# Kernel tuning notes

Measured on AMD Instinct MI355X. Metric: run time of the kernel, lower is better.

Reference implementation:

```python
import jax, jax.numpy as jnp
import numpy as np

EMB = 256
IN_CH = 256
CTX_D = 128


def setup_inputs() -> dict:
    key = jax.random.key(0)
    ks = jax.random.split(key, 12)
    b, c, h, w = 16, IN_CH, 48, 48
    seq = 2048
    s = 0.02
    return {
        "x": jax.random.normal(ks[0], (b, c, h, w), jnp.float32),
        "context": jax.random.normal(ks[1], (b, seq, CTX_D), jnp.float32),
        "pad_mask": jax.random.bernoulli(ks[2], 0.1, (b, h * w, seq)),
        "W_in": jax.random.normal(ks[3], (EMB, IN_CH), jnp.float32) * s,   # 1x1 conv weight
        "b_in": jnp.zeros((EMB,), jnp.float32),
        "Wq": jax.random.normal(ks[4], (EMB, EMB), jnp.float32) * s,
        "bq": jnp.zeros((EMB,), jnp.float32),
        "Wk": jax.random.normal(ks[5], (EMB, CTX_D), jnp.float32) * s,
        "bk": jnp.zeros((EMB,), jnp.float32),
        "Wv": jax.random.normal(ks[6], (EMB, CTX_D), jnp.float32) * s,
        "bv": jnp.zeros((EMB,), jnp.float32),
        "W_out": jax.random.normal(ks[7], (IN_CH, EMB), jnp.float32) * s,  # 1x1 conv weight
        "b_out": jnp.zeros((IN_CH,), jnp.float32),
    }


def reference(x, context, pad_mask, W_in, b_in, Wq, bq, Wk, bk, Wv, bv, W_out, b_out):
    b, c, h, w = x.shape
    scale = EMB ** (-0.5)
    # proj_in: 1x1 conv == channel matmul; then b c h w -> b (h w) c
    xt = jnp.einsum('bchw,ec->behw', x, W_in) + b_in[None, :, None, None]
    xt = xt.reshape(b, EMB, h * w).transpose(0, 2, 1)          # [b, hw, emb]
    Q = xt @ Wq.T + bq                                          # [b, hw, emb]
    K = context @ Wk.T + bk                                     # [b, seq, emb]
    V = context @ Wv.T + bv                                     # [b, seq, emb]
    att = jnp.einsum('bid,bjd->bij', Q, K) * scale              # [b, hw, seq]
    att = jnp.where(pad_mask, jnp.float32(-1e9), att)
    att = jax.nn.softmax(att, axis=-1)
    out = jnp.einsum('bij,bjd->bid', att, V)                    # [b, hw, emb]
    out = out.transpose(0, 2, 1).reshape(b, EMB, h, w)
    out = jnp.einsum('behw,ce->bchw', out, W_out) + b_out[None, :, None, None]
    return out, att
```

## Files before the change

kernel.cpp:

```cpp
#include <hip/hip_runtime.h>

typedef unsigned short u16;
typedef unsigned int   u32;
typedef __attribute__((ext_vector_type(8))) __bf16 bf16x8;
typedef __attribute__((ext_vector_type(4))) float  f32x4;

#define BB   16
#define CH   256
#define HW   2304
#define SEQ  2048
#define EMB  256
#define CTXD 128
#define OUT0 9437184
#define NQT  72
#define SLOTF 65536

#define MFMA(a,b,c) __builtin_amdgcn_mfma_f32_16x16x32_bf16(a,b,c,0,0,0)

__device__ __forceinline__ u16 f2bf(float f){
  u32 u = __builtin_bit_cast(u32, f);
  u += 0x7fffu + ((u >> 16) & 1u);
  return (u16)(u >> 16);
}
__device__ __forceinline__ float bf2f(u32 us){ return __builtin_bit_cast(float, us << 16); }

__device__ __forceinline__ bf16x8 ld16(const u16* p){
  uint4 q = *reinterpret_cast<const uint4*>(p);
  return __builtin_bit_cast(bf16x8, q);
}
__device__ __forceinline__ bf16x8 mk8(float a0,float a1,float a2,float a3,
                                      float a4,float a5,float a6,float a7){
  uint4 q;
  q.x = (u32)f2bf(a0) | ((u32)f2bf(a1) << 16);
  q.y = (u32)f2bf(a2) | ((u32)f2bf(a3) << 16);
  q.z = (u32)f2bf(a4) | ((u32)f2bf(a5) << 16);
  q.w = (u32)f2bf(a6) | ((u32)f2bf(a7) << 16);
  return __builtin_bit_cast(bf16x8, q);
}

__global__ __launch_bounds__(256) void k_prep(
    const float* __restrict__ Wq, const float* __restrict__ W_in,
    const float* __restrict__ b_in, const float* __restrict__ bq,
    const float* __restrict__ Wk, const float* __restrict__ Wv,
    const float* __restrict__ Wout,
    u16* __restrict__ WqinBf, u16* __restrict__ WkBf, u16* __restrict__ WvBf,
    u16* __restrict__ WoutBf, float* __restrict__ bq_eff)
{
  int blk = blockIdx.x, t = threadIdx.x;
  if (blk < 256) {
    int e = blk, c = t;
    float s = 0.f;
    for (int f = 0; f < 256; f++) s += Wq[e*256+f] * W_in[f*256+c];
    WqinBf[e*256+c] = f2bf(s);
    if (t == 0) {
      float bb = bq[e];
      for (int f = 0; f < 256; f++) bb += Wq[e*256+f] * b_in[f];
      bq_eff[e] = bb;
    }
  } else {
    u32 flat = (u32)(blk - 256) * 256 + t;
    for (u32 idx = flat; idx < 131072u; idx += 16384u) {
      if (idx < 32768u)       WkBf[idx]          = f2bf(Wk[idx]);
      else if (idx < 65536u)  WvBf[idx - 32768u] = f2bf(Wv[idx - 32768u]);
      else                    WoutBf[idx - 65536u] = f2bf(Wout[idx - 65536u]);
    }
  }
}

__global__ __launch_bounds__(256) void k_qproj(
    const float* __restrict__ x, const u16* __restrict__ WqinBf,
    const float* __restrict__ bq_eff, u16* __restrict__ Qbf)
{
  int b = blockIdx.y, ibase = blockIdx.x * 64;
  int t = threadIdx.x, wv = t >> 6, lane = t & 63, g4 = lane >> 4, r16 = lane & 15;
  int e0 = wv * 64;
  f32x4 acc[4][4] = {};
  #pragma unroll 2
  for (int kk = 0; kk < 8; kk++) {
    bf16x8 a[4];
    #pragma unroll
    for (int m = 0; m < 4; m++)
      a[m] = ld16(WqinBf + (size_t)(e0 + m*16 + r16) * 256 + kk*32 + g4*8);
    bf16x8 bb[4];
    #pragma unroll
    for (int n = 0; n < 4; n++) {
      const float* xp = x + ((size_t)b*CH + kk*32 + g4*8) * HW + ibase + n*16 + r16;
      bb[n] = mk8(xp[0], xp[HW], xp[2*HW], xp[3*HW], xp[4*HW], xp[5*HW], xp[6*HW], xp[7*HW]);
    }
    #pragma unroll
    for (int m = 0; m < 4; m++)
      #pragma unroll
      for (int n = 0; n < 4; n++)
        acc[m][n] = MFMA(a[m], bb[n], acc[m][n]);
  }
  #pragma unroll
  for (int m = 0; m < 4; m++) {
    int e = e0 + m*16 + g4*4;
    float b0 = bq_eff[e], b1 = bq_eff[e+1], b2 = bq_eff[e+2], b3 = bq_eff[e+3];
    #pragma unroll
    for (int n = 0; n < 4; n++) {
      int i = ibase + n*16 + r16;
      u32 lo = (u32)f2bf(acc[m][n][0] + b0) | ((u32)f2bf(acc[m][n][1] + b1) << 16);
      u32 hi = (u32)f2bf(acc[m][n][2] + b2) | ((u32)f2bf(acc[m][n][3] + b3) << 16);
      *(uint2*)(Qbf + ((size_t)b*HW + i) * EMB + e) = make_uint2(lo, hi);
    }
  }
}

__global__ __launch_bounds__(512) void k_kvproj(
    const float* __restrict__ ctx, const u16* __restrict__ WkBf, const u16* __restrict__ WvBf,
    const float* __restrict__ bk, const float* __restrict__ bv,
    u16* __restrict__ Kbf, u16* __restrict__ Vtb)
{
  int b = blockIdx.y, sbase = blockIdx.x * 64;
  int t = threadIdx.x, wv = t >> 6, lane = t & 63, g4 = lane >> 4, r16 = lane & 15;
  bool isV = wv >= 4;
  int e0 = (wv & 3) * 64;
  const u16* Wsel = isV ? WvBf : WkBf;
  f32x4 acc[4][4] = {};
  #pragma unroll
  for (int kk = 0; kk < 4; kk++) {
    bf16x8 a[4];
    #pragma unroll
    for (int m = 0; m < 4; m++)
      a[m] = ld16(Wsel + (size_t)(e0 + m*16 + r16) * 128 + kk*32 + g4*8);
    bf16x8 bb[4];
    #pragma unroll
    for (int n = 0; n < 4; n++) {
      const float* cp = ctx + ((size_t)b*SEQ + sbase + n*16 + r16) * CTXD + kk*32 + g4*8;
      float4 lo = *(const float4*)cp;
      float4 hi = *(const float4*)(cp + 4);
      bb[n] = mk8(lo.x, lo.y, lo.z, lo.w, hi.x, hi.y, hi.z, hi.w);
    }
    #pragma unroll
    for (int m = 0; m < 4; m++)
      #pragma unroll
      for (int n = 0; n < 4; n++)
        acc[m][n] = MFMA(a[m], bb[n], acc[m][n]);
  }
  if (!isV) {
    #pragma unroll
    for (int m = 0; m < 4; m++) {
      int e = e0 + m*16 + g4*4;
      float b0 = bk[e], b1 = bk[e+1], b2 = bk[e+2], b3 = bk[e+3];
      #pragma unroll
      for (int n = 0; n < 4; n++) {
        int s = sbase + n*16 + r16;
        u32 lo = (u32)f2bf(acc[m][n][0] + b0) | ((u32)f2bf(acc[m][n][1] + b1) << 16);
        u32 hi = (u32)f2bf(acc[m][n][2] + b2) | ((u32)f2bf(acc[m][n][3] + b3) << 16);
        *(uint2*)(Kbf + ((size_t)b*SEQ + s) * EMB + e) = make_uint2(lo, hi);
      }
    }
  } else {
    #pragma unroll
    for (int m = 0; m < 4; m++) {
      #pragma unroll
      for (int r = 0; r < 4; r++) {
        int e = e0 + m*16 + g4*4 + r;
        float bvv = bv[e];
        #pragma unroll
        for (int n = 0; n < 4; n++) {
          int s = sbase + n*16 + r16;
          Vtb[((size_t)b*EMB + e) * SEQ + s] = f2bf(acc[m][n][r] + bvv);
        }
      }
    }
  }
}

__global__ __launch_bounds__(512) void k_attn(
    const u16* __restrict__ Qbf, const u16* __restrict__ Kbf,
    const u16* __restrict__ Vtb, const int* __restrict__ mask,
    float* __restrict__ dout, u16* __restrict__ Obf)
{
  __shared__ u16 Els[32][2048];
  __shared__ float red[8][32];
  __shared__ float invs[32];

  int b = blockIdx.y, qt = blockIdx.x, qbase = qt * 32;
  int t = threadIdx.x, wv = t >> 6, lane = t & 63, g4 = lane >> 4, r16 = lane & 15;
  int jb = wv * 256;
  int slot = b * NQT + qt;
  float* attf = dout + OUT0 + (size_t)slot * SLOTF;

  bf16x8 qf[2][8];
  #pragma unroll
  for (int m = 0; m < 2; m++) {
    const u16* qp = Qbf + ((size_t)b*HW + qbase + m*16 + r16) * EMB + g4*8;
    #pragma unroll
    for (int kk = 0; kk < 8; kk++) qf[m][kk] = ld16(qp + kk*32);
  }
  float rs[2][4] = {};
  const float SC = 0.0625f;
  #pragma unroll 1
  for (int nch = 0; nch < 4; nch++) {
    f32x4 acc[2][4] = {};
    #pragma unroll
    for (int kk = 0; kk < 8; kk++) {
      bf16x8 kf[4];
      #pragma unroll
      for (int n = 0; n < 4; n++)
        kf[n] = ld16(Kbf + ((size_t)b*SEQ + jb + nch*64 + n*16 + r16) * EMB + kk*32 + g4*8);
      #pragma unroll
      for (int m = 0; m < 2; m++)
        #pragma unroll
        for (int n = 0; n < 4; n++)
          acc[m][n] = MFMA(qf[m][kk], kf[n], acc[m][n]);
    }
    #pragma unroll
    for (int m = 0; m < 2; m++) {
      int li0 = m*16 + g4*4;
      #pragma unroll
      for (int n = 0; n < 4; n++) {
        int j = jb + nch*64 + n*16 + r16;
        const int* mp = mask + ((size_t)b*HW + qbase + li0) * SEQ + j;
        #pragma unroll
        for (int r = 0; r < 4; r++) {
          float s = acc[m][n][r] * SC;
          int mk = mp[(size_t)r * SEQ];
          float e = mk ? 0.f : __expf(s);
          rs[m][r] += e;
          int row = li0 + r;
          u32 bo = (u32)(j * 2) ^ ((u32)(row & 7) << 4);
          *(u16*)((char*)&Els[row][0] + bo) = f2bf(e);
        }
      }
    }
  }
  #pragma unroll
  for (int m = 0; m < 2; m++)
    #pragma unroll
    for (int r = 0; r < 4; r++) {
      float v = rs[m][r];
      v += __shfl_xor(v, 1); v += __shfl_xor(v, 2);
      v += __shfl_xor(v, 4); v += __shfl_xor(v, 8);
      if (r16 == 0) red[wv][m*16 + g4*4 + r] = v;
    }
  __syncthreads();
  if (t < 32) {
    float s2 = 0.f;
    #pragma unroll
    for (int w2 = 0; w2 < 8; w2++) s2 += red[w2][t];
    invs[t] = 1.f / s2;
  }
  __syncthreads();

  int e0 = wv * 32;
  const u16* Vb = Vtb + (size_t)b * EMB * SEQ;
  int arow = t >> 4;
  int acol = (t & 15) * 2;
  float ivA = invs[arow];
  const char* ErowA = (const char*)&Els[arow][0];
  u32 axor = (u32)(arow & 7) << 4;
  const char* E0p = (const char*)&Els[r16][0];
  const char* E1p = (const char*)&Els[16 + r16][0];
  u32 rxor = (u32)(r16 & 7) << 4;

  f32x4 acc2[2][2] = {};
  #pragma unroll 2
  for (int kk = 0; kk < 64; kk++) {
    int ko = kk*32 + g4*8;
    u32 bo = (u32)(ko * 2) ^ rxor;
    bf16x8 a0 = __builtin_bit_cast(bf16x8, *(const uint4*)(E0p + bo));
    bf16x8 a1 = __builtin_bit_cast(bf16x8, *(const uint4*)(E1p + bo));
    bf16x8 b0 = ld16(Vb + (size_t)(e0 + r16) * SEQ + ko);
    bf16x8 b1 = ld16(Vb + (size_t)(e0 + 16 + r16) * SEQ + ko);
    acc2[0][0] = MFMA(a0, b0, acc2[0][0]);
    acc2[0][1] = MFMA(a0, b1, acc2[0][1]);
    acc2[1][0] = MFMA(a1, b0, acc2[1][0]);
    acc2[1][1] = MFMA(a1, b1, acc2[1][1]);
    u32 abo = (u32)(kk*64 + (t & 15)*4) ^ axor;
    u32 araw = *(const u32*)(ErowA + abo);
    float2 av;
    av.x = bf2f(araw & 0xffffu) * ivA;
    av.y = bf2f(araw >> 16) * ivA;
    *(float2*)(attf + (size_t)arow * 2048 + kk*32 + acol) = av;
  }
  #pragma unroll
  for (int m = 0; m < 2; m++)
    #pragma unroll
    for (int r = 0; r < 4; r++) {
      int li = m*16 + g4*4 + r;
      float iv = invs[li];
      #pragma unroll
      for (int n = 0; n < 2; n++)
        Obf[((size_t)b*HW + qbase + li) * EMB + e0 + n*16 + r16] = f2bf(acc2[m][n][r] * iv);
    }
}

__global__ __launch_bounds__(256) void k_outproj(
    const u16* __restrict__ Obf, const u16* __restrict__ WoutBf,
    const float* __restrict__ bout, float* __restrict__ out)
{
  int b = blockIdx.y, ibase = blockIdx.x * 64;
  int t = threadIdx.x, wv = t >> 6, lane = t & 63, g4 = lane >> 4, r16 = lane & 15;
  int c0 = wv * 64;
  f32x4 acc[4][4] = {};
  #pragma unroll 2
  for (int kk = 0; kk < 8; kk++) {
    bf16x8 a[4];
    #pragma unroll
    for (int m = 0; m < 4; m++)
      a[m] = ld16(WoutBf + (size_t)(c0 + m*16 + r16) * 256 + kk*32 + g4*8);
    bf16x8 bb[4];
    #pragma unroll
    for (int n = 0; n < 4; n++)
      bb[n] = ld16(Obf + ((size_t)b*HW + ibase + n*16 + r16) * EMB + kk*32 + g4*8);
    #pragma unroll
    for (int m = 0; m < 4; m++)
      #pragma unroll
      for (int n = 0; n < 4; n++)
        acc[m][n] = MFMA(a[m], bb[n], acc[m][n]);
  }
  #pragma unroll
  for (int m = 0; m < 4; m++) {
    #pragma unroll
    for (int r = 0; r < 4; r++) {
      int c = c0 + m*16 + g4*4 + r;
      float bo = bout[c];
      #pragma unroll
      for (int n = 0; n < 4; n++) {
        int i = ibase + n*16 + r16;
        out[((size_t)b*CH + c) * HW + i] = acc[m][n][r] + bo;
      }
    }
  }
}

extern "C" void kernel_launch(void* const* d_in, const int* in_sizes, int n_in,
                              void* d_out, int out_size, void* d_ws, size_t ws_size,
                              hipStream_t stream)
{
  const float* x    = (const float*)d_in[0];
  const float* ctx  = (const float*)d_in[1];
  const int*   mask = (const int*)  d_in[2];
  const float* W_in = (const float*)d_in[3];
  const float* b_in = (const float*)d_in[4];
  const float* Wq   = (const float*)d_in[5];
  const float* bq   = (const float*)d_in[6];
  const float* Wk   = (const float*)d_in[7];
  const float* bk   = (const float*)d_in[8];
  const float* Wv   = (const float*)d_in[9];
  const float* bv   = (const float*)d_in[10];
  const float* Wout = (const float*)d_in[11];
  const float* bout = (const float*)d_in[12];
  float* out = (float*)d_out;

  char* ws = (char*)d_ws;
  size_t off = 0;
  auto alloc = [&](size_t bytes) -> void* {
    void* p = ws + off;
    off += (bytes + 255) & ~(size_t)255;
    return p;
  };
  u16*   WqinBf = (u16*)  alloc(256*256*2);
  u16*   WkBf   = (u16*)  alloc(256*128*2);
  u16*   WvBf   = (u16*)  alloc(256*128*2);
  u16*   WoutBf = (u16*)  alloc(256*256*2);
  float* bq_eff = (float*)alloc(256*4);
  u16*   Qbf    = (u16*)  alloc((size_t)BB*HW*EMB*2);
  u16*   Kbf    = (u16*)  alloc((size_t)BB*SEQ*EMB*2);
  u16*   Vtb    = (u16*)  alloc((size_t)BB*EMB*SEQ*2);
  if (off > ws_size) return;

  k_prep<<<dim3(320), dim3(256), 0, stream>>>(Wq, W_in, b_in, bq, Wk, Wv, Wout,
                                              WqinBf, WkBf, WvBf, WoutBf, bq_eff);
  k_qproj<<<dim3(36, 16), dim3(256), 0, stream>>>(x, WqinBf, bq_eff, Qbf);
  k_kvproj<<<dim3(32, 16), dim3(512), 0, stream>>>(ctx, WkBf, WvBf, bk, bv, Kbf, Vtb);
  k_attn<<<dim3(NQT, 16), dim3(512), 0, stream>>>(Qbf, Kbf, Vtb, mask, out, Qbf );
  k_outproj<<<dim3(36, 16), dim3(256), 0, stream>>>(Qbf , WoutBf, bout, out);
}
```

Measured before the change: 502.3 us.

## Pack mask to bits and split attention across 1024-thread blocks

Adds a pre-pass that compresses the int32 pad mask into 64-bit ballot words, so the attention kernel reads bitmasks instead of strided int loads. The attention kernel now runs 16 waves per block, with each wave covering half as many keys and output columns. Q is reloaded per k-step rather than held in registers, and the normalized attention-matrix writeback moves after the PV loop as wide float4 stores. The extra pass still reads the full mask once, and the 1024-thread blocks may limit occupancy.

```diff
diff --git a/kernel.cpp b/kernel.cpp
--- a/kernel.cpp
+++ b/kernel.cpp
@@ -2,6 +2,7 @@
 
 typedef unsigned short u16;
 typedef unsigned int   u32;
+typedef unsigned long long u64;
 typedef __attribute__((ext_vector_type(8))) __bf16 bf16x8;
 typedef __attribute__((ext_vector_type(4))) float  f32x4;
 
@@ -14,6 +15,7 @@
 #define OUT0 9437184
 #define NQT  72
 #define SLOTF 65536
+#define NMASKW 1179648u
 
 #define MFMA(a,b,c) __builtin_amdgcn_mfma_f32_16x16x32_bf16(a,b,c,0,0,0)
 
@@ -67,6 +69,19 @@
   }
 }
 
+__global__ __launch_bounds__(256) void k_maskpack(
+    const int* __restrict__ mask, u64* __restrict__ mb)
+{
+  u32 wid = ((u32)blockIdx.x * 256u + (u32)threadIdx.x) >> 6;
+  u32 lane = threadIdx.x & 63;
+  u32 nwv = ((u32)gridDim.x * 256u) >> 6;
+  for (u32 w = wid; w < NMASKW; w += nwv) {
+    int m = mask[(size_t)w * 64 + lane];
+    u64 bm = __ballot(m != 0);
+    if (lane == 0) mb[w] = bm;
+  }
+}
+
 __global__ __launch_bounds__(256) void k_qproj(
     const float* __restrict__ x, const u16* __restrict__ WqinBf,
     const float* __restrict__ bq_eff, u16* __restrict__ Qbf)
@@ -168,56 +183,60 @@
   }
 }
 
-__global__ __launch_bounds__(512) void k_attn(
+__global__ __launch_bounds__(1024) void k_attn(
     const u16* __restrict__ Qbf, const u16* __restrict__ Kbf,
-    const u16* __restrict__ Vtb, const int* __restrict__ mask,
+    const u16* __restrict__ Vtb, const u32* __restrict__ mb,
     float* __restrict__ dout, u16* __restrict__ Obf)
 {
   __shared__ u16 Els[32][2048];
-  __shared__ float red[8][32];
+  __shared__ float red[16][32];
   __shared__ float invs[32];
 
   int b = blockIdx.y, qt = blockIdx.x, qbase = qt * 32;
   int t = threadIdx.x, wv = t >> 6, lane = t & 63, g4 = lane >> 4, r16 = lane & 15;
-  int jb = wv * 256;
-  int slot = b * NQT + qt;
-  float* attf = dout + OUT0 + (size_t)slot * SLOTF;
-
-  bf16x8 qf[2][8];
-  #pragma unroll
-  for (int m = 0; m < 2; m++) {
-    const u16* qp = Qbf + ((size_t)b*HW + qbase + m*16 + r16) * EMB + g4*8;
-    #pragma unroll
-    for (int kk = 0; kk < 8; kk++) qf[m][kk] = ld16(qp + kk*32);
-  }
+  int jb = wv * 128;
+  float* attf = dout + OUT0 + (size_t)(b * NQT + qt) * SLOTF;
+  const u32* mrow = mb + ((size_t)b * HW + qbase) * 64;
+  const u16* Qrow = Qbf + ((size_t)b * HW + qbase) * EMB;
+  const u16* Krow = Kbf + (size_t)b * SEQ * EMB;
+
   float rs[2][4] = {};
   const float SC = 0.0625f;
-  #pragma unroll 1
-  for (int nch = 0; nch < 4; nch++) {
+  #pragma unroll
+  for (int nch = 0; nch < 2; nch++) {
+    int jbase = jb + nch * 64;
+    uint2 mw[2][4];
+    #pragma unroll
+    for (int m = 0; m < 2; m++)
+      #pragma unroll
+      for (int r = 0; r < 4; r++)
+        mw[m][r] = *(const uint2*)(mrow + (size_t)(m*16 + g4*4 + r) * 64 + (jbase >> 5));
     f32x4 acc[2][4] = {};
     #pragma unroll
     for (int kk = 0; kk < 8; kk++) {
       bf16x8 kf[4];
       #pragma unroll
       for (int n = 0; n < 4; n++)
-        kf[n] = ld16(Kbf + ((size_t)b*SEQ + jb + nch*64 + n*16 + r16) * EMB + kk*32 + g4*8);
-      #pragma unroll
-      for (int m = 0; m < 2; m++)
-        #pragma unroll
-        for (int n = 0; n < 4; n++)
-          acc[m][n] = MFMA(qf[m][kk], kf[n], acc[m][n]);
+        kf[n] = ld16(Krow + (size_t)(jbase + n*16 + r16) * EMB + kk*32 + g4*8);
+      bf16x8 q0 = ld16(Qrow + (size_t)(r16) * EMB + kk*32 + g4*8);
+      bf16x8 q1 = ld16(Qrow + (size_t)(16 + r16) * EMB + kk*32 + g4*8);
+      #pragma unroll
+      for (int n = 0; n < 4; n++) {
+        acc[0][n] = MFMA(q0, kf[n], acc[0][n]);
+        acc[1][n] = MFMA(q1, kf[n], acc[1][n]);
+      }
     }
     #pragma unroll
     for (int m = 0; m < 2; m++) {
       int li0 = m*16 + g4*4;
       #pragma unroll
       for (int n = 0; n < 4; n++) {
-        int j = jb + nch*64 + n*16 + r16;
-        const int* mp = mask + ((size_t)b*HW + qbase + li0) * SEQ + j;
+        int j = jbase + n*16 + r16;
         #pragma unroll
         for (int r = 0; r < 4; r++) {
+          u32 wbits = (n < 2) ? mw[m][r].x : mw[m][r].y;
+          u32 mk = (wbits >> ((n & 1) * 16 + r16)) & 1u;
           float s = acc[m][n][r] * SC;
-          int mk = mp[(size_t)r * SEQ];
           float e = mk ? 0.f : __expf(s);
           rs[m][r] += e;
           int row = li0 + r;
@@ -240,52 +259,52 @@
   if (t < 32) {
     float s2 = 0.f;
     #pragma unroll
-    for (int w2 = 0; w2 < 8; w2++) s2 += red[w2][t];
+    for (int w2 = 0; w2 < 16; w2++) s2 += red[w2][t];
     invs[t] = 1.f / s2;
   }
   __syncthreads();
 
-  int e0 = wv * 32;
-  const u16* Vb = Vtb + (size_t)b * EMB * SEQ;
-  int arow = t >> 4;
-  int acol = (t & 15) * 2;
-  float ivA = invs[arow];
-  const char* ErowA = (const char*)&Els[arow][0];
-  u32 axor = (u32)(arow & 7) << 4;
+  int e0 = wv * 16;
+  const u16* Vb = Vtb + (size_t)b * EMB * SEQ + (size_t)(e0 + r16) * SEQ;
   const char* E0p = (const char*)&Els[r16][0];
   const char* E1p = (const char*)&Els[16 + r16][0];
   u32 rxor = (u32)(r16 & 7) << 4;
-
-  f32x4 acc2[2][2] = {};
-  #pragma unroll 2
+  f32x4 acc2[2] = {};
+  #pragma unroll 4
   for (int kk = 0; kk < 64; kk++) {
     int ko = kk*32 + g4*8;
     u32 bo = (u32)(ko * 2) ^ rxor;
     bf16x8 a0 = __builtin_bit_cast(bf16x8, *(const uint4*)(E0p + bo));
     bf16x8 a1 = __builtin_bit_cast(bf16x8, *(const uint4*)(E1p + bo));
-    bf16x8 b0 = ld16(Vb + (size_t)(e0 + r16) * SEQ + ko);
-    bf16x8 b1 = ld16(Vb + (size_t)(e0 + 16 + r16) * SEQ + ko);
-    acc2[0][0] = MFMA(a0, b0, acc2[0][0]);
-    acc2[0][1] = MFMA(a0, b1, acc2[0][1]);
-    acc2[1][0] = MFMA(a1, b0, acc2[1][0]);
-    acc2[1][1] = MFMA(a1, b1, acc2[1][1]);
-    u32 abo = (u32)(kk*64 + (t & 15)*4) ^ axor;
-    u32 araw = *(const u32*)(ErowA + abo);
-    float2 av;
-    av.x = bf2f(araw & 0xffffu) * ivA;
-    av.y = bf2f(araw >> 16) * ivA;
-    *(float2*)(attf + (size_t)arow * 2048 + kk*32 + acol) = av;
+    bf16x8 b0 = ld16(Vb + ko);
+    acc2[0] = MFMA(a0, b0, acc2[0]);
+    acc2[1] = MFMA(a1, b0, acc2[1]);
   }
   #pragma unroll
   for (int m = 0; m < 2; m++)
     #pragma unroll
     for (int r = 0; r < 4; r++) {
       int li = m*16 + g4*4 + r;
-      float iv = invs[li];
-      #pragma unroll
-      for (int n = 0; n < 2; n++)
-        Obf[((size_t)b*HW + qbase + li) * EMB + e0 + n*16 + r16] = f2bf(acc2[m][n][r] * iv);
-    }
+      Obf[((size_t)b*HW + qbase + li) * EMB + e0 + r16] = f2bf(acc2[m][r] * invs[li]);
+    }
+
+  int arow = t >> 5;
+  int ac = (t & 31) * 4;
+  float ivA = invs[arow];
+  const char* ErowA = (const char*)&Els[arow][0];
+  u32 axor = (u32)(arow & 7) << 4;
+  float* attr = attf + (size_t)arow * 2048;
+  #pragma unroll 2
+  for (int it = 0; it < 16; it++) {
+    int col = it * 128 + ac;
+    uint2 raw = *(const uint2*)(ErowA + ((u32)(col * 2) ^ axor));
+    float4 o;
+    o.x = bf2f(raw.x & 0xffffu) * ivA;
+    o.y = bf2f(raw.x >> 16) * ivA;
+    o.z = bf2f(raw.y & 0xffffu) * ivA;
+    o.w = bf2f(raw.y >> 16) * ivA;
+    *(float4*)(attr + col) = o;
+  }
 }
 
 __global__ __launch_bounds__(256) void k_outproj(
@@ -358,6 +377,7 @@
   u16*   WvBf   = (u16*)  alloc(256*128*2);
   u16*   WoutBf = (u16*)  alloc(256*256*2);
   float* bq_eff = (float*)alloc(256*4);
+  u64*   mbits  = (u64*)  alloc((size_t)NMASKW*8);
   u16*   Qbf    = (u16*)  alloc((size_t)BB*HW*EMB*2);
   u16*   Kbf    = (u16*)  alloc((size_t)BB*SEQ*EMB*2);
   u16*   Vtb    = (u16*)  alloc((size_t)BB*EMB*SEQ*2);
@@ -365,8 +385,10 @@
 
   k_prep<<<dim3(320), dim3(256), 0, stream>>>(Wq, W_in, b_in, bq, Wk, Wv, Wout,
                                               WqinBf, WkBf, WvBf, WoutBf, bq_eff);
+  k_maskpack<<<dim3(2048), dim3(256), 0, stream>>>(mask, mbits);
   k_qproj<<<dim3(36, 16), dim3(256), 0, stream>>>(x, WqinBf, bq_eff, Qbf);
   k_kvproj<<<dim3(32, 16), dim3(512), 0, stream>>>(ctx, WkBf, WvBf, bk, bv, Kbf, Vtb);
-  k_attn<<<dim3(NQT, 16), dim3(512), 0, stream>>>(Qbf, Kbf, Vtb, mask, out, Qbf );
+  k_attn<<<dim3(NQT, 16), dim3(1024), 0, stream>>>(Qbf, Kbf, Vtb, (const u32*)mbits,
+                                                   out, Qbf );
   k_outproj<<<dim3(36, 16), dim3(256), 0, stream>>>(Qbf , WoutBf, bout, out);
 }
```

Result: slower. 722.3 us (+43.8%).

## Halve attention query tile to 16 rows and remap blocks for occupancy

Applied to the files above, without the earlier changes.

The attention kernel now handles 16 query rows per block instead of 32, doubling the grid to 2304 one-dimensional blocks and halving LDS use so up to four blocks can share a CU (launch_bounds 512,4). Block IDs are interleaved so that neighbouring blocks map to different batches and query tiles. The attention-probability writeback moves after the PV matmul and uses float4 stores per row instead of float2 stores interleaved with the MFMA loop. The trade is that each K and V tile is now reused across fewer query rows, so K/V global reads double.

```diff
diff --git a/kernel.cpp b/kernel.cpp
--- a/kernel.cpp
+++ b/kernel.cpp
@@ -2,6 +2,7 @@
 
 typedef unsigned short u16;
 typedef unsigned int   u32;
+typedef unsigned long long u64;
 typedef __attribute__((ext_vector_type(8))) __bf16 bf16x8;
 typedef __attribute__((ext_vector_type(4))) float  f32x4;
 
@@ -12,8 +13,9 @@
 #define EMB  256
 #define CTXD 128
 #define OUT0 9437184
-#define NQT  72
-#define SLOTF 65536
+#define QROWS 16
+#define NQT  144
+#define NBLK 2304
 
 #define MFMA(a,b,c) __builtin_amdgcn_mfma_f32_16x16x32_bf16(a,b,c,0,0,0)
 
@@ -168,76 +170,72 @@
   }
 }
 
-__global__ __launch_bounds__(512) void k_attn(
+__global__ __launch_bounds__(512, 4) void k_attn(
     const u16* __restrict__ Qbf, const u16* __restrict__ Kbf,
     const u16* __restrict__ Vtb, const int* __restrict__ mask,
     float* __restrict__ dout, u16* __restrict__ Obf)
 {
-  __shared__ u16 Els[32][2048];
-  __shared__ float red[8][32];
-  __shared__ float invs[32];
-
-  int b = blockIdx.y, qt = blockIdx.x, qbase = qt * 32;
+  __shared__ u16 Els[QROWS][2048];
+  __shared__ float red[8][QROWS];
+  __shared__ float invs[QROWS];
+
+  int bid = blockIdx.x;
+  int work = (bid & 7) * (NBLK / 8) + (bid >> 3);
+  int b = work / NQT, qt = work % NQT;
+  int qbase = qt * QROWS;
+
   int t = threadIdx.x, wv = t >> 6, lane = t & 63, g4 = lane >> 4, r16 = lane & 15;
   int jb = wv * 256;
-  int slot = b * NQT + qt;
-  float* attf = dout + OUT0 + (size_t)slot * SLOTF;
-
-  bf16x8 qf[2][8];
-  #pragma unroll
-  for (int m = 0; m < 2; m++) {
-    const u16* qp = Qbf + ((size_t)b*HW + qbase + m*16 + r16) * EMB + g4*8;
-    #pragma unroll
-    for (int kk = 0; kk < 8; kk++) qf[m][kk] = ld16(qp + kk*32);
-  }
-  float rs[2][4] = {};
+  const u16* Qrow = Qbf + ((size_t)b * HW + qbase) * EMB;
+  const u16* Krow = Kbf + (size_t)b * SEQ * EMB;
+  const int* mrow = mask + ((size_t)b * HW + qbase + g4*4) * SEQ;
+
+  bf16x8 qf[8];
+  #pragma unroll
+  for (int kk = 0; kk < 8; kk++)
+    qf[kk] = ld16(Qrow + (size_t)r16 * EMB + kk*32 + g4*8);
+
+  float rs[4] = {};
   const float SC = 0.0625f;
   #pragma unroll 1
   for (int nch = 0; nch < 4; nch++) {
-    f32x4 acc[2][4] = {};
+    int jbase = jb + nch * 64;
+    f32x4 acc[4] = {};
     #pragma unroll
     for (int kk = 0; kk < 8; kk++) {
       bf16x8 kf[4];
       #pragma unroll
       for (int n = 0; n < 4; n++)
-        kf[n] = ld16(Kbf + ((size_t)b*SEQ + jb + nch*64 + n*16 + r16) * EMB + kk*32 + g4*8);
-      #pragma unroll
-      for (int m = 0; m < 2; m++)
-        #pragma unroll
-        for (int n = 0; n < 4; n++)
-          acc[m][n] = MFMA(qf[m][kk], kf[n], acc[m][n]);
-    }
-    #pragma unroll
-    for (int m = 0; m < 2; m++) {
-      int li0 = m*16 + g4*4;
-      #pragma unroll
-      for (int n = 0; n < 4; n++) {
-        int j = jb + nch*64 + n*16 + r16;
-        const int* mp = mask + ((size_t)b*HW + qbase + li0) * SEQ + j;
-        #pragma unroll
-        for (int r = 0; r < 4; r++) {
-          float s = acc[m][n][r] * SC;
-          int mk = mp[(size_t)r * SEQ];
-          float e = mk ? 0.f : __expf(s);
-          rs[m][r] += e;
-          int row = li0 + r;
-          u32 bo = (u32)(j * 2) ^ ((u32)(row & 7) << 4);
-          *(u16*)((char*)&Els[row][0] + bo) = f2bf(e);
-        }
+        kf[n] = ld16(Krow + (size_t)(jbase + n*16 + r16) * EMB + kk*32 + g4*8);
+      #pragma unroll
+      for (int n = 0; n < 4; n++)
+        acc[n] = MFMA(qf[kk], kf[n], acc[n]);
+    }
+    #pragma unroll
+    for (int n = 0; n < 4; n++) {
+      int j = jbase + n*16 + r16;
+      const int* mp = mrow + j;
+      #pragma unroll
+      for (int r = 0; r < 4; r++) {
+        float s = acc[n][r] * SC;
+        int mk = mp[(size_t)r * SEQ];
+        float e = mk ? 0.f : __expf(s);
+        rs[r] += e;
+        int row = g4*4 + r;
+        u32 bo = (u32)(j * 2) ^ ((u32)(row & 7) << 4);
+        *(u16*)((char*)&Els[row][0] + bo) = f2bf(e);
       }
     }
   }
   #pragma unroll
-  for (int m = 0; m < 2; m++)
-    #pragma unroll
-    for (int r = 0; r < 4; r++) {
-      float v = rs[m][r];
-      v += __shfl_xor(v, 1); v += __shfl_xor(v, 2);
-      v += __shfl_xor(v, 4); v += __shfl_xor(v, 8);
-      if (r16 == 0) red[wv][m*16 + g4*4 + r] = v;
-    }
+  for (int r = 0; r < 4; r++) {
+    float v = rs[r];
+    v += __shfl_xor(v, 1); v += __shfl_xor(v, 2);
+    v += __shfl_xor(v, 4); v += __shfl_xor(v, 8);
+    if (r16 == 0) red[wv][g4*4 + r] = v;
+  }
   __syncthreads();
-  if (t < 32) {
+  if (t < QROWS) {
     float s2 = 0.f;
     #pragma unroll
     for (int w2 = 0; w2 < 8; w2++) s2 += red[w2][t];
@@ -247,45 +245,46 @@
 
   int e0 = wv * 32;
   const u16* Vb = Vtb + (size_t)b * EMB * SEQ;
-  int arow = t >> 4;
-  int acol = (t & 15) * 2;
-  float ivA = invs[arow];
-  const char* ErowA = (const char*)&Els[arow][0];
-  u32 axor = (u32)(arow & 7) << 4;
   const char* E0p = (const char*)&Els[r16][0];
-  const char* E1p = (const char*)&Els[16 + r16][0];
   u32 rxor = (u32)(r16 & 7) << 4;
-
-  f32x4 acc2[2][2] = {};
-  #pragma unroll 2
+  f32x4 acc2[2] = {};
+  #pragma unroll 4
   for (int kk = 0; kk < 64; kk++) {
     int ko = kk*32 + g4*8;
     u32 bo = (u32)(ko * 2) ^ rxor;
     bf16x8 a0 = __builtin_bit_cast(bf16x8, *(const uint4*)(E0p + bo));
-    bf16x8 a1 = __builtin_bit_cast(bf16x8, *(const uint4*)(E1p + bo));
     bf16x8 b0 = ld16(Vb + (size_t)(e0 + r16) * SEQ + ko);
     bf16x8 b1 = ld16(Vb + (size_t)(e0 + 16 + r16) * SEQ + ko);
-    acc2[0][0] = MFMA(a0, b0, acc2[0][0]);
-    acc2[0][1] = MFMA(a0, b1, acc2[0][1]);
-    acc2[1][0] = MFMA(a1, b0, acc2[1][0]);
-    acc2[1][1] = MFMA(a1, b1, acc2[1][1]);
-    u32 abo = (u32)(kk*64 + (t & 15)*4) ^ axor;
-    u32 araw = *(const u32*)(ErowA + abo);
-    float2 av;
-    av.x = bf2f(araw & 0xffffu) * ivA;
-    av.y = bf2f(araw >> 16) * ivA;
-    *(float2*)(attf + (size_t)arow * 2048 + kk*32 + acol) = av;
-  }
-  #pragma unroll
-  for (int m = 0; m < 2; m++)
-    #pragma unroll
-    for (int r = 0; r < 4; r++) {
-      int li = m*16 + g4*4 + r;
-      float iv = invs[li];
-      #pragma unroll
-      for (int n = 0; n < 2; n++)
-        Obf[((size_t)b*HW + qbase + li) * EMB + e0 + n*16 + r16] = f2bf(acc2[m][n][r] * iv);
-    }
+    acc2[0] = MFMA(a0, b0, acc2[0]);
+    acc2[1] = MFMA(a0, b1, acc2[1]);
+  }
+  #pragma unroll
+  for (int r = 0; r < 4; r++) {
+    int li = g4*4 + r;
+    float iv = invs[li];
+    #pragma unroll
+    for (int n = 0; n < 2; n++)
+      Obf[((size_t)b*HW + qbase + li) * EMB + e0 + n*16 + r16] = f2bf(acc2[n][r] * iv);
+  }
+
+  float* attf = dout + OUT0 + (size_t)(b * HW + qbase) * SEQ;
+  int arow = t >> 5;
+  int ac = (t & 31) * 4;
+  float ivA = invs[arow];
+  const char* ErowA = (const char*)&Els[arow][0];
+  u32 axor = (u32)(arow & 7) << 4;
+  float* attr = attf + (size_t)arow * 2048;
+  #pragma unroll 2
+  for (int it = 0; it < 16; it++) {
+    int col = it * 128 + ac;
+    uint2 raw = *(const uint2*)(ErowA + ((u32)(col * 2) ^ axor));
+    float4 o;
+    o.x = bf2f(raw.x & 0xffffu) * ivA;
+    o.y = bf2f(raw.x >> 16) * ivA;
+    o.z = bf2f(raw.y & 0xffffu) * ivA;
+    o.w = bf2f(raw.y >> 16) * ivA;
+    *(float4*)(attr + col) = o;
+  }
 }
 
 __global__ __launch_bounds__(256) void k_outproj(
@@ -367,6 +366,6 @@
                                               WqinBf, WkBf, WvBf, WoutBf, bq_eff);
   k_qproj<<<dim3(36, 16), dim3(256), 0, stream>>>(x, WqinBf, bq_eff, Qbf);
   k_kvproj<<<dim3(32, 16), dim3(512), 0, stream>>>(ctx, WkBf, WvBf, bk, bv, Kbf, Vtb);
-  k_attn<<<dim3(NQT, 16), dim3(512), 0, stream>>>(Qbf, Kbf, Vtb, mask, out, Qbf );
+  k_attn<<<dim3(NBLK), dim3(512), 0, stream>>>(Qbf, Kbf, Vtb, mask, out, Qbf );
   k_outproj<<<dim3(36, 16), dim3(256), 0, stream>>>(Qbf , WoutBf, bout, out);
 }
```

After: 759.8 us. 51.3% more time.
